# Kernel tuning notes

Hardware: AMD Instinct MI355X
Metric: run time of the kernel (lower is better)

The kernel has to match this reference:

```python
import jax, jax.numpy as jnp
import numpy as np
from jax import lax

EPS = 0.1
MAX_ITER = 100
THRESH = 0.01
N = 4  # number of prompt ensembles


def _l2norm(x, axis):
    return x / jnp.linalg.norm(x, axis=axis, keepdims=True)


def sinkhorn(K, u, v, max_iter=MAX_ITER, thresh=THRESH):
    # K: [B, M, N], u: [B, M], v: [B, N]. Matches torch loop with early exit
    # on mean(|r - r0|) < thresh, done on-device via lax.while_loop.
    dt = K.dtype
    r0 = jnp.ones_like(u)
    c0 = jnp.ones_like(v)

    def cond(state):
        _, _, i, err = state
        return jnp.logical_and(i < max_iter, err >= thresh)

    def body(state):
        r, c, i, _ = state
        r_new = u / jnp.einsum('bmn,bn->bm', K, c)
        c_new = v / jnp.einsum('bmn,bm->bn', K, r_new)
        err = jnp.mean(jnp.abs(r_new - r))
        return (r_new, c_new, i + 1, err)

    r, c, _, _ = lax.while_loop(cond, body, (r0, c0, jnp.int32(0), jnp.asarray(jnp.inf, dt)))
    # T = outer(r, c) * K
    return r[:, :, None] * c[:, None, :] * K


def setup_inputs() -> dict:
    key = jax.random.key(0)
    k1, k2, k3 = jax.random.split(key, 3)
    M, b, d = 196, 32, 512
    n_cls = 1000
    return {
        'image_features': jax.random.normal(k1, (M, b, d), dtype=jnp.float32),
        'image_feature_pool': jax.random.normal(k2, (b, d), dtype=jnp.float32),
        'text_features': jax.random.normal(k3, (N * n_cls, d), dtype=jnp.float32),
        'logit_scale': jnp.asarray(np.log(1.0 / 0.07), dtype=jnp.float32),
    }


def reference(image_features, image_feature_pool, text_features, logit_scale):
    M, b, d = image_features.shape
    n_cls = text_features.shape[0] // N

    tf = text_features.reshape(N, n_cls, d)
    text_feature_pool = tf.mean(axis=0)

    imf = _l2norm(image_features, axis=2)          # [M, b, d]
    img_pool = _l2norm(image_feature_pool, axis=1)  # [b, d]
    tfn = _l2norm(tf, axis=2)                       # [N, n_cls, d]
    txt_pool = _l2norm(text_feature_pool, axis=1)   # [n_cls, d]

    # sim: [M, N, b, n_cls] -> [M, N, b*n_cls] -> [B, M, N]
    sim = jnp.einsum('mbd,ncd->mnbc', imf, tfn)
    sim = sim.reshape(M, N, b * n_cls).transpose(2, 0, 1)
    wdist = 1.0 - sim

    B = b * n_cls
    xx = jnp.full((B, M), 1.0 / M, dtype=sim.dtype)
    yy = jnp.full((B, N), 1.0 / N, dtype=sim.dtype)

    # torch.no_grad() around Sinkhorn -> stop gradients into the iteration
    K = jnp.exp(-lax.stop_gradient(wdist) / EPS)
    T = sinkhorn(K, xx, yy)

    sim_op = jnp.sum(T * sim, axis=(1, 2)).reshape(b, n_cls)

    ls = jnp.exp(logit_scale)
    logits = ls * (img_pool @ txt_pool.T)
    logits2 = 0.5 * (ls * sim_op) + 0.5 * logits
    return logits2
```

## Files before the change

kernel.cpp:

```cpp
#include <hip/hip_runtime.h>
#include <hip/hip_bf16.h>

#define MB 6272
#define NC 4000
#define DD 512
#define NCLS 1000
#define NB 32000
#define NITER 6
#define SK_STRIDE 132

typedef __attribute__((ext_vector_type(8))) short short8;
typedef __attribute__((ext_vector_type(4))) float f32x4;
typedef __attribute__((ext_vector_type(2))) float f32x2;

__device__ __forceinline__ float bflo(unsigned u) { return __builtin_bit_cast(float, u << 16); }
__device__ __forceinline__ float bfhi(unsigned u) { return __builtin_bit_cast(float, u & 0xFFFF0000u); }
__device__ __forceinline__ float frcp(float x) { return __builtin_amdgcn_rcpf(x); }

__device__ __forceinline__ unsigned short f2bf(float x) {
  unsigned u = __builtin_bit_cast(unsigned, x);
  u += 0x7FFFu + ((u >> 16) & 1u);
  return (unsigned short)(u >> 16);
}

__device__ __forceinline__ bool is_fp32_mode(const void* lsp) {
  const unsigned short u = *(const unsigned short*)lsp;
  const float v = __builtin_bit_cast(float, (unsigned)u << 16);
  return !(v > 2.55f && v < 2.77f);
}

__device__ __forceinline__ void gl_lds16(const unsigned short* g, unsigned short* l) {
  __builtin_amdgcn_global_load_lds(
      (const __attribute__((address_space(1))) void*)g,
      (__attribute__((address_space(3))) void*)l, 16, 0, 0);
}

__global__ __launch_bounds__(256) void prep(const void* __restrict__ imgf,
                                            const void* __restrict__ imgp,
                                            const void* __restrict__ txtf,
                                            const void* __restrict__ lsp,
                                            float* __restrict__ rnAT, float* __restrict__ rnB,
                                            float* __restrict__ imgpool,
                                            float* __restrict__ txtpool,
                                            unsigned short* __restrict__ Ab,
                                            unsigned short* __restrict__ Bb) {
  const bool f32 = is_fp32_mode(lsp);
  const int w = threadIdx.x >> 6;
  const int lane = threadIdx.x & 63;
  const int row = blockIdx.x * 4 + w;
  const int d0 = lane * 8;

  float v[8];
  auto load8f = [&](const void* base, int srow) {
    if (f32) {
      const float4 a = *reinterpret_cast<const float4*>((const float*)base + (size_t)srow * DD + d0);
      const float4 b = *reinterpret_cast<const float4*>((const float*)base + (size_t)srow * DD + d0 + 4);
      v[0] = a.x; v[1] = a.y; v[2] = a.z; v[3] = a.w;
      v[4] = b.x; v[5] = b.y; v[6] = b.z; v[7] = b.w;
    } else {
      const uint4 u = *reinterpret_cast<const uint4*>((const unsigned short*)base + (size_t)srow * DD + d0);
      v[0] = bflo(u.x); v[1] = bfhi(u.x); v[2] = bflo(u.y); v[3] = bfhi(u.y);
      v[4] = bflo(u.z); v[5] = bfhi(u.z); v[6] = bflo(u.w); v[7] = bfhi(u.w);
    }
  };

  int mode;
  unsigned short* dst16 = nullptr;
  float* dstf = nullptr;
  int outidx = 0;
  if (row < MB) {
    load8f(imgf, row); mode = 0; dst16 = Ab + (size_t)row * DD + d0;
    outidx = (row & 31) * 208 + (row >> 5);
  } else if (row < MB + NC) {
    const int j = row - MB;
    load8f(txtf, (j & 3) * NCLS + (j >> 2)); mode = 1;
    dst16 = Bb + (size_t)j * DD + d0; outidx = j;
  } else if (row < MB + NC + 32) {
    const int b = row - MB - NC;
    load8f(imgp, b); mode = 2; dstf = imgpool + (size_t)b * DD + d0;
  } else {
    const int cc = row - (MB + NC + 32);
    float acc8[8] = {0, 0, 0, 0, 0, 0, 0, 0};
#pragma unroll
    for (int n = 0; n < 4; ++n) {
      load8f(txtf, n * NCLS + cc);
#pragma unroll
      for (int i = 0; i < 8; ++i) acc8[i] += v[i];
    }
#pragma unroll
    for (int i = 0; i < 8; ++i) v[i] = acc8[i] * 0.25f;
    mode = 3; dstf = txtpool + (size_t)cc * DD + d0;
  }

  float ss = 0.f;
#pragma unroll
  for (int i = 0; i < 8; ++i) ss += v[i] * v[i];
#pragma unroll
  for (int off = 1; off < 64; off <<= 1) ss += __shfl_xor(ss, off);
  const float rn = rsqrtf(ss);

  if (mode <= 1) {
    union { uint4 u; unsigned short h[8]; } r;
#pragma unroll
    for (int i = 0; i < 8; ++i) r.h[i] = f2bf(v[i]);
    *reinterpret_cast<uint4*>(dst16) = r.u;
    if (lane == 0) (mode == 0 ? rnAT : rnB)[outidx] = rn;
  } else {
    float4 a, b;
    a.x = v[0] * rn; a.y = v[1] * rn; a.z = v[2] * rn; a.w = v[3] * rn;
    b.x = v[4] * rn; b.y = v[5] * rn; b.z = v[6] * rn; b.w = v[7] * rn;
    *reinterpret_cast<float4*>(dstf) = a;
    *reinterpret_cast<float4*>(dstf + 4) = b;
  }
}

__global__ __launch_bounds__(256, 3) void gemm_sink(const unsigned short* __restrict__ Ab,
                                                    const unsigned short* __restrict__ Bb,
                                                    const float* __restrict__ rnAT,
                                                    const float* __restrict__ rnB,
                                                    const float* __restrict__ imgpool,
                                                    const float* __restrict__ txtpool,
                                                    const void* __restrict__ lsp,
                                                    void* __restrict__ out) {
  __shared__ unsigned short shm[196 * SK_STRIDE];
  __shared__ float rnAs[208];
  unsigned short* Asx = shm;
  unsigned short* Bsx = shm + 6656;

  const int t = threadIdx.x;
  const int lane = t & 63;
  const int w = t >> 6;
  const int b = blockIdx.x;
  const int y = blockIdx.y;
  const int quad = lane >> 4, l16 = lane & 15;

  if (t < 208) rnAs[t] = rnAT[b * 208 + t];

  f32x4 acc[13][2];
#pragma unroll
  for (int mt = 0; mt < 13; ++mt) {
    acc[mt][0] = (f32x4)0.f;
    acc[mt][1] = (f32x4)0.f;
  }

  for (int k0 = 0; k0 < DD; k0 += 32) {
#pragma unroll
    for (int r = 0; r < 3; ++r) {
      const int g = r * 256 + t;
      const int rr = g >> 2;
      const int seg = g & 3;
      const int sg = (seg ^ (rr & 3)) * 8;
      gl_lds16(Ab + (size_t)(rr * 32 + b) * DD + k0 + sg,
               Asx + (size_t)(r * 256 + w * 64) * 8);
    }
    if (w == 0) {
      const int rr = 192 + (lane >> 2);
      const int seg = lane & 3;
      const int sg = (seg ^ (rr & 3)) * 8;
      const int arow = rr < 196 ? rr : 195;
      gl_lds16(Ab + (size_t)(arow * 32 + b) * DD + k0 + sg, Asx + (size_t)768 * 8);
    }
#pragma unroll
    for (int r = 0; r < 2; ++r) {
      const int g = r * 256 + t;
      const int rr = g >> 2;
      const int seg = g & 3;
      const int sg = (seg ^ (rr & 3)) * 8;
      const int jg0 = y * 128 + rr;
      const int jg = jg0 < NC ? jg0 : NC - 1;
      gl_lds16(Bb + (size_t)jg * DD + k0 + sg, Bsx + (size_t)(r * 256 + w * 64) * 8);
    }
    __syncthreads();
    short8 bfr[2];
#pragma unroll
    for (int ct = 0; ct < 2; ++ct) {
      const int rw = w * 32 + ct * 16 + l16;
      bfr[ct] = *reinterpret_cast<const short8*>(&Bsx[rw * 32 + (quad ^ (rw & 3)) * 8]);
    }
#pragma unroll
    for (int mt = 0; mt < 13; ++mt) {
      const int rw = mt * 16 + l16;
      const short8 af = *reinterpret_cast<const short8*>(&Asx[rw * 32 + (quad ^ (rw & 3)) * 8]);
      acc[mt][0] = __builtin_amdgcn_mfma_f32_16x16x32_bf16(af, bfr[0], acc[mt][0], 0, 0, 0);
      acc[mt][1] = __builtin_amdgcn_mfma_f32_16x16x32_bf16(af, bfr[1], acc[mt][1], 0, 0, 0);
    }
    __syncthreads();
  }

#pragma unroll
  for (int mt = 0; mt < 13; ++mt) {
#pragma unroll
    for (int ct = 0; ct < 2; ++ct) {
      const int jl = w * 32 + ct * 16 + l16;
      const int jg = y * 128 + jl;
      const float rb = jg < NC ? rnB[jg] : 1.0f;
#pragma unroll
      for (int reg = 0; reg < 4; ++reg) {
        const int m = mt * 16 + quad * 4 + reg;
        if (m < 196) {
          const float sim = acc[mt][ct][reg] * rnAs[m] * rb;
          shm[m * SK_STRIDE + jl] = f2bf(__expf(10.f * sim - 10.f));
        }
      }
    }
  }
  __syncthreads();

  const int pl = lane >> 3;
  const int sub = lane & 7;
  const int mstart = sub < 4 ? sub * 25 : 100 + (sub - 4) * 24;
  const int pcol = (w * 8 + pl) * 4;

  uint2 kk[25];
#pragma unroll
  for (int i = 0; i < 25; ++i) {
    const int m = mstart + i;
    const int mc = m < 196 ? m : 195;
    kk[i] = *reinterpret_cast<const uint2*>(&shm[mc * SK_STRIDE + pcol]);
  }

  f32x2 cA = {1.f, 1.f}, cB = {1.f, 1.f};
  for (int it = 0; it < NITER - 1; ++it) {
    f32x2 SA = {0.f, 0.f}, SB = {0.f, 0.f};
#pragma unroll
    for (int i = 0; i < 25; ++i) {
      if (i < 24 || sub < 4) {
        f32x2 kA = {bflo(kk[i].x), bfhi(kk[i].x)};
        f32x2 kB = {bflo(kk[i].y), bfhi(kk[i].y)};
        const f32x2 pr = kA * cA + kB * cB;
        const float rv = (1.0f / 196.0f) * frcp(pr.x + pr.y);
        const f32x2 rvv = {rv, rv};
        SA += kA * rvv;
        SB += kB * rvv;
      }
    }
    SA.x += __shfl_xor(SA.x, 1); SA.x += __shfl_xor(SA.x, 2); SA.x += __shfl_xor(SA.x, 4);
    SA.y += __shfl_xor(SA.y, 1); SA.y += __shfl_xor(SA.y, 2); SA.y += __shfl_xor(SA.y, 4);
    SB.x += __shfl_xor(SB.x, 1); SB.x += __shfl_xor(SB.x, 2); SB.x += __shfl_xor(SB.x, 4);
    SB.y += __shfl_xor(SB.y, 1); SB.y += __shfl_xor(SB.y, 2); SB.y += __shfl_xor(SB.y, 4);
    cA.x = 0.25f * frcp(SA.x); cA.y = 0.25f * frcp(SA.y);
    cB.x = 0.25f * frcp(SB.x); cB.y = 0.25f * frcp(SB.y);
  }

  f32x2 SA = {0.f, 0.f}, SB = {0.f, 0.f}, WA = {0.f, 0.f}, WB = {0.f, 0.f};
#pragma unroll
  for (int i = 0; i < 25; ++i) {
    if (i < 24 || sub < 4) {
      f32x2 kA = {bflo(kk[i].x), bfhi(kk[i].x)};
      f32x2 kB = {bflo(kk[i].y), bfhi(kk[i].y)};
      const f32x2 pr = kA * cA + kB * cB;
      const float rv = (1.0f / 196.0f) * frcp(pr.x + pr.y);
      const f32x2 rvv = {rv, rv};
      const f32x2 tA = kA * rvv, tB = kB * rvv;
      SA += tA; SB += tB;
      const f32x2 lgA = {__logf(kA.x), __logf(kA.y)};
      const f32x2 lgB = {__logf(kB.x), __logf(kB.y)};
      const f32x2 one = {1.f, 1.f}, tenth = {0.1f, 0.1f};
      WA += tA * (one + tenth * lgA);
      WB += tB * (one + tenth * lgB);
    }
  }
  SA.x += __shfl_xor(SA.x, 1); SA.x += __shfl_xor(SA.x, 2); SA.x += __shfl_xor(SA.x, 4);
  SA.y += __shfl_xor(SA.y, 1); SA.y += __shfl_xor(SA.y, 2); SA.y += __shfl_xor(SA.y, 4);
  SB.x += __shfl_xor(SB.x, 1); SB.x += __shfl_xor(SB.x, 2); SB.x += __shfl_xor(SB.x, 4);
  SB.y += __shfl_xor(SB.y, 1); SB.y += __shfl_xor(SB.y, 2); SB.y += __shfl_xor(SB.y, 4);
  WA.x += __shfl_xor(WA.x, 1); WA.x += __shfl_xor(WA.x, 2); WA.x += __shfl_xor(WA.x, 4);
  WA.y += __shfl_xor(WA.y, 1); WA.y += __shfl_xor(WA.y, 2); WA.y += __shfl_xor(WA.y, 4);
  WB.x += __shfl_xor(WB.x, 1); WB.x += __shfl_xor(WB.x, 2); WB.x += __shfl_xor(WB.x, 4);
  WB.y += __shfl_xor(WB.y, 1); WB.y += __shfl_xor(WB.y, 2); WB.y += __shfl_xor(WB.y, 4);
  const float simop = (0.25f * frcp(SA.x)) * WA.x + (0.25f * frcp(SA.y)) * WA.y +
                      (0.25f * frcp(SB.x)) * WB.x + (0.25f * frcp(SB.y)) * WB.y;

  const int cg = y * 32 + (w * 8 + pl);
  const int cgc = cg < NCLS ? cg : NCLS - 1;
  const float4* ip4 = reinterpret_cast<const float4*>(imgpool + (size_t)b * DD);
  const float4* tp4 = reinterpret_cast<const float4*>(txtpool + (size_t)cgc * DD);
  float dot = 0.f;
#pragma unroll
  for (int i = 0; i < 16; ++i) {
    const float4 a = ip4[sub * 16 + i];
    const float4 v = tp4[sub * 16 + i];
    dot += (a.x * v.x + a.y * v.y) + (a.z * v.z + a.w * v.w);
  }
  dot += __shfl_xor(dot, 1); dot += __shfl_xor(dot, 2); dot += __shfl_xor(dot, 4);

  if (sub == 0 && cg < NCLS) {
    const bool f32 = is_fp32_mode(lsp);
    const float lsv = f32 ? *(const float*)lsp : bflo(*(const unsigned short*)lsp);
    const float val = 0.5f * __expf(lsv) * (simop + dot);
    const int p = b * NCLS + cg;
    if (f32) ((float*)out)[p] = val;
    else ((unsigned short*)out)[p] = f2bf(val);
  }
}

extern "C" void kernel_launch(void* const* d_in, const int* in_sizes, int n_in,
                              void* d_out, int out_size, void* d_ws, size_t ws_size,
                              hipStream_t stream) {
  const void* imgf = d_in[0];
  const void* imgp = d_in[1];
  const void* txtf = d_in[2];
  const void* lsp  = d_in[3];

  const size_t need = (size_t)32 * 208 * 4 + NC * 4 + 32 * DD * 4 + NCLS * DD * 4 +
                      (size_t)MB * DD * 2 + (size_t)NC * DD * 2;
  const bool ok = (n_in == 4) && in_sizes[0] == MB * DD && in_sizes[1] == 32 * DD &&
                  in_sizes[2] == NC * DD && in_sizes[3] == 1 && out_size == NB &&
                  ws_size >= need;
  if (!ok) return;

  char* w = (char*)d_ws;
  float* rnAT = (float*)w;                 w += (size_t)32 * 208 * 4;
  float* rnB = (float*)w;                  w += NC * 4;
  float* imgpool = (float*)w;              w += 32 * DD * 4;
  float* txtpool = (float*)w;              w += NCLS * DD * 4;
  unsigned short* Ab = (unsigned short*)w; w += (size_t)MB * DD * 2;
  unsigned short* Bb = (unsigned short*)w; w += (size_t)NC * DD * 2;

  prep<<<dim3(2826), dim3(256), 0, stream>>>(imgf, imgp, txtf, lsp, rnAT, rnB,
                                             imgpool, txtpool, Ab, Bb);
  gemm_sink<<<dim3(32, 32), dim3(256), 0, stream>>>(Ab, Bb, rnAT, rnB, imgpool,
                                                    txtpool, lsp, d_out);
}
```

Measured before the change: 142.5 us.

## Load B fragments directly to registers with prefetch, widen K-step to 64, pre-unpack K

New measurement: 167.2 us. 17.3% more time.

```diff
diff --git a/kernel.cpp b/kernel.cpp
--- a/kernel.cpp
+++ b/kernel.cpp
@@ -125,7 +125,6 @@
   __shared__ unsigned short shm[196 * SK_STRIDE];
   __shared__ float rnAs[208];
   unsigned short* Asx = shm;
-  unsigned short* Bsx = shm + 6656;
 
   const int t = threadIdx.x;
   const int lane = t & 63;
@@ -143,48 +142,64 @@
     acc[mt][1] = (f32x4)0.f;
   }
 
-  for (int k0 = 0; k0 < DD; k0 += 32) {
-#pragma unroll
-    for (int r = 0; r < 3; ++r) {
+  const unsigned short* Brow[2];
+#pragma unroll
+  for (int ct = 0; ct < 2; ++ct) {
+    int jg = y * 128 + w * 32 + ct * 16 + l16;
+    jg = jg < NC ? jg : NC - 1;
+    Brow[ct] = Bb + (size_t)jg * DD + quad * 8;
+  }
+
+  short8 bcur[2][2], bnext[2][2];
+#pragma unroll
+  for (int ct = 0; ct < 2; ++ct)
+#pragma unroll
+    for (int kh = 0; kh < 2; ++kh)
+      bcur[ct][kh] = *reinterpret_cast<const short8*>(Brow[ct] + kh * 32);
+
+  for (int s = 0; s < 8; ++s) {
+    const int k0 = s * 64;
+#pragma unroll
+    for (int r = 0; r < 6; ++r) {
       const int g = r * 256 + t;
-      const int rr = g >> 2;
-      const int seg = g & 3;
-      const int sg = (seg ^ (rr & 3)) * 8;
-      gl_lds16(Ab + (size_t)(rr * 32 + b) * DD + k0 + sg,
-               Asx + (size_t)(r * 256 + w * 64) * 8);
-    }
-    if (w == 0) {
-      const int rr = 192 + (lane >> 2);
-      const int seg = lane & 3;
-      const int sg = (seg ^ (rr & 3)) * 8;
+      const int rr = g >> 3;
+      const int seg = g & 7;
+      const int sg = (seg ^ (rr & 7)) * 8;
+      gl_lds16(Ab + (size_t)(rr * 32 + b) * DD + k0 + sg, Asx + (size_t)g * 8);
+    }
+    if (w < 2) {
+      const int g = 1536 + w * 64 + lane;
+      const int rr = g >> 3;
+      const int seg = g & 7;
+      const int sg = (seg ^ (rr & 7)) * 8;
       const int arow = rr < 196 ? rr : 195;
-      gl_lds16(Ab + (size_t)(arow * 32 + b) * DD + k0 + sg, Asx + (size_t)768 * 8);
-    }
-#pragma unroll
-    for (int r = 0; r < 2; ++r) {
-      const int g = r * 256 + t;
-      const int rr = g >> 2;
-      const int seg = g & 3;
-      const int sg = (seg ^ (rr & 3)) * 8;
-      const int jg0 = y * 128 + rr;
-      const int jg = jg0 < NC ? jg0 : NC - 1;
-      gl_lds16(Bb + (size_t)jg * DD + k0 + sg, Bsx + (size_t)(r * 256 + w * 64) * 8);
+      gl_lds16(Ab + (size_t)(arow * 32 + b) * DD + k0 + sg,
+               Asx + (size_t)(1536 + w * 64) * 8);
     }
     __syncthreads();
-    short8 bfr[2];
-#pragma unroll
-    for (int ct = 0; ct < 2; ++ct) {
-      const int rw = w * 32 + ct * 16 + l16;
-      bfr[ct] = *reinterpret_cast<const short8*>(&Bsx[rw * 32 + (quad ^ (rw & 3)) * 8]);
+    if (s < 7) {
+#pragma unroll
+      for (int ct = 0; ct < 2; ++ct)
+#pragma unroll
+        for (int kh = 0; kh < 2; ++kh)
+          bnext[ct][kh] = *reinterpret_cast<const short8*>(Brow[ct] + k0 + 64 + kh * 32);
     }
 #pragma unroll
     for (int mt = 0; mt < 13; ++mt) {
       const int rw = mt * 16 + l16;
-      const short8 af = *reinterpret_cast<const short8*>(&Asx[rw * 32 + (quad ^ (rw & 3)) * 8]);
-      acc[mt][0] = __builtin_amdgcn_mfma_f32_16x16x32_bf16(af, bfr[0], acc[mt][0], 0, 0, 0);
-      acc[mt][1] = __builtin_amdgcn_mfma_f32_16x16x32_bf16(af, bfr[1], acc[mt][1], 0, 0, 0);
+      const short8 af0 = *reinterpret_cast<const short8*>(&Asx[rw * 64 + (quad ^ (rw & 7)) * 8]);
+      const short8 af1 = *reinterpret_cast<const short8*>(&Asx[rw * 64 + ((4 + quad) ^ (rw & 7)) * 8]);
+      acc[mt][0] = __builtin_amdgcn_mfma_f32_16x16x32_bf16(af0, bcur[0][0], acc[mt][0], 0, 0, 0);
+      acc[mt][0] = __builtin_amdgcn_mfma_f32_16x16x32_bf16(af1, bcur[0][1], acc[mt][0], 0, 0, 0);
+      acc[mt][1] = __builtin_amdgcn_mfma_f32_16x16x32_bf16(af0, bcur[1][0], acc[mt][1], 0, 0, 0);
+      acc[mt][1] = __builtin_amdgcn_mfma_f32_16x16x32_bf16(af1, bcur[1][1], acc[mt][1], 0, 0, 0);
     }
     __syncthreads();
+#pragma unroll
+    for (int ct = 0; ct < 2; ++ct)
+#pragma unroll
+      for (int kh = 0; kh < 2; ++kh)
+        bcur[ct][kh] = bnext[ct][kh];
   }
 
 #pragma unroll
@@ -211,12 +226,14 @@
   const int mstart = sub < 4 ? sub * 25 : 100 + (sub - 4) * 24;
   const int pcol = (w * 8 + pl) * 4;
 
-  uint2 kk[25];
+  f32x2 kAf[25], kBf[25];
 #pragma unroll
   for (int i = 0; i < 25; ++i) {
     const int m = mstart + i;
     const int mc = m < 196 ? m : 195;
-    kk[i] = *reinterpret_cast<const uint2*>(&shm[mc * SK_STRIDE + pcol]);
+    const uint2 u = *reinterpret_cast<const uint2*>(&shm[mc * SK_STRIDE + pcol]);
+    kAf[i].x = bflo(u.x); kAf[i].y = bfhi(u.x);
+    kBf[i].x = bflo(u.y); kBf[i].y = bfhi(u.y);
   }
 
   f32x2 cA = {1.f, 1.f}, cB = {1.f, 1.f};
@@ -225,13 +242,11 @@
 #pragma unroll
     for (int i = 0; i < 25; ++i) {
       if (i < 24 || sub < 4) {
-        f32x2 kA = {bflo(kk[i].x), bfhi(kk[i].x)};
-        f32x2 kB = {bflo(kk[i].y), bfhi(kk[i].y)};
-        const f32x2 pr = kA * cA + kB * cB;
+        const f32x2 pr = kAf[i] * cA + kBf[i] * cB;
         const float rv = (1.0f / 196.0f) * frcp(pr.x + pr.y);
         const f32x2 rvv = {rv, rv};
-        SA += kA * rvv;
-        SB += kB * rvv;
+        SA += kAf[i] * rvv;
+        SB += kBf[i] * rvv;
       }
     }
     SA.x += __shfl_xor(SA.x, 1); SA.x += __shfl_xor(SA.x, 2); SA.x += __shfl_xor(SA.x, 4);
@@ -246,15 +261,13 @@
 #pragma unroll
   for (int i = 0; i < 25; ++i) {
     if (i < 24 || sub < 4) {
-      f32x2 kA = {bflo(kk[i].x), bfhi(kk[i].x)};
-      f32x2 kB = {bflo(kk[i].y), bfhi(kk[i].y)};
-      const f32x2 pr = kA * cA + kB * cB;
+      const f32x2 pr = kAf[i] * cA + kBf[i] * cB;
       const float rv = (1.0f / 196.0f) * frcp(pr.x + pr.y);
       const f32x2 rvv = {rv, rv};
-      const f32x2 tA = kA * rvv, tB = kB * rvv;
+      const f32x2 tA = kAf[i] * rvv, tB = kBf[i] * rvv;
       SA += tA; SB += tB;
-      const f32x2 lgA = {__logf(kA.x), __logf(kA.y)};
-      const f32x2 lgB = {__logf(kB.x), __logf(kB.y)};
+      const f32x2 lgA = {__logf(kAf[i].x), __logf(kAf[i].y)};
+      const f32x2 lgB = {__logf(kBf[i].x), __logf(kBf[i].y)};
       const f32x2 one = {1.f, 1.f}, tenth = {0.1f, 0.1f};
       WA += tA * (one + tenth * lgA);
       WB += tB * (one + tenth * lgB);
```
